# Kernel optimization log

Measured on AMD Instinct MI355X. Metric: run time of the kernel, lower is better.

## Reference

```python
import jax, jax.numpy as jnp
import numpy as np

B, S, D, H, MLP = 2, 2048, 1024, 16, 4096
DH = D // H
EPS_LN = 1e-6
KERNEL_EPS = 1e-3  # fast_attention generalized kernel_epsilon


def layer_norm(x, scale, bias):
    m = jnp.mean(x, axis=-1, keepdims=True)
    v = jnp.mean(jnp.square(x - m), axis=-1, keepdims=True)
    return (x - m) * jax.lax.rsqrt(v + EPS_LN) * scale + bias


def performer_causal_attention(q, k, v):
    """FAVOR+ generalized attention (deterministic relu features), causal.

    q,k,v: [B,S,H,DH]. phi(x) = relu(x) + eps. Linear-time via prefix sums:
      out_i = phi(q_i) . cumsum_j<=i phi(k_j) v_j^T / (phi(q_i) . cumsum phi(k_j))
    """
    phi_q = jax.nn.relu(q) + KERNEL_EPS          # [B,S,H,M]
    phi_k = jax.nn.relu(k) + KERNEL_EPS          # [B,S,H,M]
    kv = jnp.cumsum(jnp.einsum('bshm,bshd->bshmd', phi_k, v), axis=1)  # [B,S,H,M,DH]
    num = jnp.einsum('bshm,bshmd->bshd', phi_q, kv)
    den = jnp.einsum('bshm,bshm->bsh', phi_q, jnp.cumsum(phi_k, axis=1))
    return num / den[..., None]


def setup_inputs() -> dict:
    key = jax.random.key(0)
    ks = jax.random.split(key, 7)
    def w(k, shape, scale):
        return jax.random.normal(k, shape, jnp.float32) * scale
    s_in = 1.0 / np.sqrt(D)
    return {
        'inputs': jax.random.normal(ks[0], (B, S, D), jnp.float32),
        'ln1_scale': jnp.ones((D,), jnp.float32),
        'ln1_bias': jnp.zeros((D,), jnp.float32),
        'wq': w(ks[1], (D, H, DH), s_in),
        'wk': w(ks[2], (D, H, DH), s_in),
        'wv': w(ks[3], (D, H, DH), s_in),
        'wo': w(ks[4], (H, DH, D), s_in),
        'ln2_scale': jnp.ones((D,), jnp.float32),
        'ln2_bias': jnp.zeros((D,), jnp.float32),
        'w1': w(ks[5], (D, MLP), s_in),
        'b1': jnp.zeros((MLP,), jnp.float32),
        'w2': w(ks[6], (MLP, D), 1.0 / np.sqrt(MLP)),
        'b2': jnp.zeros((D,), jnp.float32),
    }


def reference(inputs, ln1_scale, ln1_bias, wq, wk, wv, wo,
              ln2_scale, ln2_bias, w1, b1, w2, b2):
    # pre-LN self-attention (Performer FAVOR+ generalized, causal)
    x = layer_norm(inputs, ln1_scale, ln1_bias)
    q = jnp.einsum('bsd,dhm->bshm', x, wq)
    k = jnp.einsum('bsd,dhm->bshm', x, wk)
    v = jnp.einsum('bsd,dhm->bshm', x, wv)
    attn = performer_causal_attention(q, k, v)          # [B,S,H,DH]
    attn_out = jnp.einsum('bshm,hmd->bsd', attn, wo)    # output projection
    x = attn_out + inputs                               # residual
    # pre-LN MLP block
    y = layer_norm(x, ln2_scale, ln2_bias)
    y = jax.nn.gelu(y @ w1 + b1) @ w2 + b2
    return x + y
```

## Files before the change

### kernel.cpp

```cpp
#include <hip/hip_runtime.h>
#include <math.h>
#include <stdint.h>

typedef __bf16 bf16;
typedef bf16  bf16x8 __attribute__((ext_vector_type(8)));
typedef float f32x4  __attribute__((ext_vector_type(4)));

constexpr int Bb  = 2;
constexpr int Ss  = 2048;
constexpr int Dd  = 1024;
constexpr int Hh  = 16;
constexpr int DHh = 64;
constexpr int MLPd = 4096;
constexpr int ROWS = Bb * Ss;
constexpr int NC  = Ss / 64;
constexpr int BH  = Bb * Hh;
constexpr float EPS_LN = 1e-6f;
constexpr float KEPS   = 1e-3f;

__device__ __forceinline__ void async_copy16(const bf16* g, bf16* l) {
    __builtin_amdgcn_global_load_lds(
        (__attribute__((address_space(1))) void*)g,
        (__attribute__((address_space(3))) void*)l,
        16, 0, 0);
}

__device__ __forceinline__ int swz64(int row, int col) {
    return row * 64 + (((col >> 3) ^ row) & 7) * 8 + (col & 7);
}

template <typename T>
__global__ __launch_bounds__(256) void ln_kernel(const T* __restrict__ x,
                                                 const float* __restrict__ scale,
                                                 const float* __restrict__ bias,
                                                 bf16* __restrict__ out)
{
    const int row = blockIdx.x;
    const T* xr = x + (size_t)row * Dd;
    const int c0 = threadIdx.x * 4;
    float vals[4];
    float sum = 0.f, sumsq = 0.f;
#pragma unroll
    for (int i = 0; i < 4; i++) {
        float v = (float)xr[c0 + i];
        vals[i] = v;
        sum += v;
        sumsq += v * v;
    }
#pragma unroll
    for (int off = 32; off > 0; off >>= 1) {
        sum   += __shfl_down(sum, off);
        sumsq += __shfl_down(sumsq, off);
    }
    __shared__ float ssum[4], ssq[4];
    const int wave = threadIdx.x >> 6;
    if ((threadIdx.x & 63) == 0) { ssum[wave] = sum; ssq[wave] = sumsq; }
    __syncthreads();
    const float tot   = ssum[0] + ssum[1] + ssum[2] + ssum[3];
    const float totsq = ssq[0] + ssq[1] + ssq[2] + ssq[3];
    const float mean = tot * (1.f / Dd);
    const float var  = totsq * (1.f / Dd) - mean * mean;
    const float r = rsqrtf(var + EPS_LN);
    bf16* orow = out + (size_t)row * Dd;
#pragma unroll
    for (int i = 0; i < 4; i++)
        orow[c0 + i] = (bf16)((vals[i] - mean) * r * scale[c0 + i] + bias[c0 + i]);
}

__global__ __launch_bounds__(256) void convert_T(const float* __restrict__ in,
                                                 bf16* __restrict__ out,
                                                 int K, int N)
{
    __shared__ float tile[32][33];
    const int k0 = blockIdx.y * 32, n0 = blockIdx.x * 32;
    const int tx = threadIdx.x & 31, ty = threadIdx.x >> 5;
#pragma unroll
    for (int i = 0; i < 32; i += 8)
        tile[ty + i][tx] = in[(size_t)(k0 + ty + i) * N + n0 + tx];
    __syncthreads();
#pragma unroll
    for (int i = 0; i < 32; i += 8)
        out[(size_t)(n0 + ty + i) * K + k0 + tx] = (bf16)tile[tx][ty + i];
}

__global__ __launch_bounds__(256) void convert_T4(const float* __restrict__ s0,
                                                  const float* __restrict__ s1,
                                                  const float* __restrict__ s2,
                                                  const float* __restrict__ s3,
                                                  bf16* __restrict__ d0,
                                                  bf16* __restrict__ d1,
                                                  bf16* __restrict__ d2,
                                                  bf16* __restrict__ d3)
{
    const float* in  = (blockIdx.z == 0) ? s0 : (blockIdx.z == 1) ? s1
                     : (blockIdx.z == 2) ? s2 : s3;
    bf16* out        = (blockIdx.z == 0) ? d0 : (blockIdx.z == 1) ? d1
                     : (blockIdx.z == 2) ? d2 : d3;
    __shared__ float tile[32][33];
    const int k0 = blockIdx.y * 32, n0 = blockIdx.x * 32;
    const int tx = threadIdx.x & 31, ty = threadIdx.x >> 5;
#pragma unroll
    for (int i = 0; i < 32; i += 8)
        tile[ty + i][tx] = in[(size_t)(k0 + ty + i) * 1024 + n0 + tx];
    __syncthreads();
#pragma unroll
    for (int i = 0; i < 32; i += 8)
        out[(size_t)(n0 + ty + i) * 1024 + k0 + tx] = (bf16)tile[tx][ty + i];
}

enum { EP_QKV = 0, EP_NONE = 1, EP_RES = 2, EP_GELU = 3, EP_BIAS_RES = 4 };

template <int TN, int BK, int NDIM, int KDIM, int MODE>
__global__ __launch_bounds__(256) void mfma_gemm(const bf16* __restrict__ A,
                                                 const bf16* __restrict__ BT,
                                                 void* __restrict__ Cout,
                                                 const float* __restrict__ bias,
                                                 const void* __restrict__ res,
                                                 bf16* __restrict__ out2,
                                                 bf16* __restrict__ out3)
{
    constexpr int WCT = TN / 2;
    constexpr int NJ  = TN / 32;
    constexpr int NS  = BK / 32;
    constexpr int CPR = BK / 8;
    constexpr int RPI = 2048 / BK;
    constexpr int GRIDY = 32;
    constexpr int RPX = GRIDY / 8;
    __shared__ bf16 As[128 * BK];
    __shared__ bf16 Bs[TN * BK];
    const int t = threadIdx.x;
    const int wave = t >> 6, lane = t & 63;

    const int bid = blockIdx.x;
    const int xcd = bid & 7, idx = bid >> 3;
    const int row0 = (xcd * RPX + (idx & (RPX - 1))) * 128;
    const int col0 = (idx / RPX) * TN;

    const int wr = wave >> 1, wc = wave & 1;

    const int srow = t / CPR;
    const int gch  = (t % CPR) ^ (srow & 7);
    const int sdst = t * 8;

    const bf16* gA = A  + (size_t)(row0 + srow) * KDIM + gch * 8;
    const bf16* gB = BT + (size_t)(col0 + srow) * KDIM + gch * 8;

    const int m = lane & 15, quad = lane >> 4;
    const int mx7 = m & 7;

    f32x4 acc[4][NJ] = {};

    for (int k0 = 0; k0 < KDIM; k0 += BK) {
        __syncthreads();
#pragma unroll
        for (int i = 0; i < 128 / RPI; i++)
            async_copy16(gA + (size_t)i * RPI * KDIM, &As[i * 2048 + sdst]);
#pragma unroll
        for (int i = 0; i < TN / RPI; i++)
            async_copy16(gB + (size_t)i * RPI * KDIM, &Bs[i * 2048 + sdst]);
        __syncthreads();

#pragma unroll
        for (int s = 0; s < NS; s++) {
            const int pco = ((s * 4 + quad) ^ mx7) * 8;
            bf16x8 aF[4], bF[NJ];
#pragma unroll
            for (int i = 0; i < 4; i++)
                aF[i] = *(const bf16x8*)&As[(wr * 64 + i * 16 + m) * BK + pco];
#pragma unroll
            for (int j = 0; j < NJ; j++)
                bF[j] = *(const bf16x8*)&Bs[(wc * WCT + j * 16 + m) * BK + pco];
#pragma unroll
            for (int i = 0; i < 4; i++)
#pragma unroll
                for (int j = 0; j < NJ; j++)
                    acc[i][j] = __builtin_amdgcn_mfma_f32_16x16x32_bf16(
                        aF[i], bF[j], acc[i][j], 0, 0, 0);
        }
        gA += BK;
        gB += BK;
    }

    bf16* qkv_dst = nullptr;
    int col_base = col0;
    bool do_phi = false;
    if constexpr (MODE == EP_QKV) {
        const int third = col0 >> 10;
        qkv_dst = (third == 0) ? (bf16*)Cout : (third == 1) ? out2 : out3;
        col_base = col0 & 1023;
        do_phi = (third < 2);
    }

#pragma unroll
    for (int i = 0; i < 4; i++) {
#pragma unroll
        for (int j = 0; j < NJ; j++) {
#pragma unroll
            for (int r = 0; r < 4; r++) {
                const int row = row0 + wr * 64 + i * 16 + quad * 4 + r;
                const int col = col0 + wc * WCT + j * 16 + m;
                float val = acc[i][j][r];
                if constexpr (MODE == EP_QKV) {
                    const int lc = col_base + wc * WCT + j * 16 + m;
                    if (do_phi) val = fmaxf(val, 0.f) + KEPS;
                    qkv_dst[(size_t)row * 1024 + lc] = (bf16)val;
                } else if constexpr (MODE == EP_NONE) {
                    ((bf16*)Cout)[(size_t)row * NDIM + col] = (bf16)val;
                } else if constexpr (MODE == EP_RES) {
                    val += ((const float*)res)[(size_t)row * NDIM + col];
                    ((bf16*)Cout)[(size_t)row * NDIM + col] = (bf16)val;
                } else if constexpr (MODE == EP_GELU) {
                    val += bias[col];
                    const float u = 0.7978845608028654f * (val + 0.044715f * val * val * val);
                    const float e = __expf(2.f * u);
                    val = val * (1.f - 1.f / (e + 1.f));
                    ((bf16*)Cout)[(size_t)row * NDIM + col] = (bf16)val;
                } else {
                    val += bias[col] + (float)((const bf16*)res)[(size_t)row * NDIM + col];
                    ((float*)Cout)[(size_t)row * NDIM + col] = val;
                }
            }
        }
    }
}

__global__ __launch_bounds__(256) void chunk_kv_kernel(const bf16* __restrict__ phik,
                                                       const bf16* __restrict__ v,
                                                       bf16* __restrict__ kvs,
                                                       float* __restrict__ ksums)
{
    const int c = blockIdx.x, bh = blockIdx.y;
    const int b = bh >> 4, h = bh & 15;
    __shared__ bf16 Kt[64 * 64];
    __shared__ bf16 Vt[64 * 64];
    const int t = threadIdx.x;
    const int wave = t >> 6, lane = t & 63;
    const int m16 = lane & 15, quad = lane >> 4;
    const int wr = wave >> 1, wc = wave & 1;
    const int f = t & 63, s4 = t >> 6;

#pragma unroll
    for (int i = 0; i < 16; i++) {
        const int s = s4 + 4 * i;
        const size_t g = ((size_t)((b * Ss + c * 64 + s) * Hh + h)) * DHh + f;
        Kt[swz64(f, s)] = phik[g];
        Vt[swz64(f, s)] = v[g];
    }
    __syncthreads();

    f32x4 acc[2][2] = {};
#pragma unroll
    for (int ks = 0; ks < 2; ks++) {
        bf16x8 aF[2], bF[2];
#pragma unroll
        for (int i = 0; i < 2; i++)
            aF[i] = *(const bf16x8*)&Kt[swz64(wr * 32 + i * 16 + m16, ks * 32 + quad * 8)];
#pragma unroll
        for (int j = 0; j < 2; j++)
            bF[j] = *(const bf16x8*)&Vt[swz64(wc * 32 + j * 16 + m16, ks * 32 + quad * 8)];
#pragma unroll
        for (int i = 0; i < 2; i++)
#pragma unroll
            for (int j = 0; j < 2; j++)
                acc[i][j] = __builtin_amdgcn_mfma_f32_16x16x32_bf16(
                    aF[i], bF[j], acc[i][j], 0, 0, 0);
    }

    const size_t base = ((size_t)bh * NC + c) * 4096;
#pragma unroll
    for (int i = 0; i < 2; i++)
#pragma unroll
        for (int j = 0; j < 2; j++)
#pragma unroll
            for (int r = 0; r < 4; r++) {
                const int mrow = wr * 32 + i * 16 + quad * 4 + r;
                const int dcol = wc * 32 + j * 16 + m16;
                kvs[base + mrow * 64 + dcol] = (bf16)acc[i][j][r];
            }

    if (t < 64) {
        float s_ = 0.f;
#pragma unroll
        for (int p = 0; p < 8; p++) {
            bf16x8 k8 = *(const bf16x8*)&Kt[t * 64 + p * 8];
#pragma unroll
            for (int e = 0; e < 8; e++) s_ += (float)k8[e];
        }
        ksums[((size_t)bh * NC + c) * 64 + t] = s_;
    }
}

__global__ __launch_bounds__(256) void scan_kernel(bf16* __restrict__ kvs,
                                                   float* __restrict__ ksums)
{
    const int e  = blockIdx.x * 256 + threadIdx.x;
    const int bh = blockIdx.y;
    float run = 0.f;
#pragma unroll 4
    for (int c = 0; c < NC; c++) {
        const size_t idx = ((size_t)bh * NC + c) * 4096 + e;
        const float val = (float)kvs[idx];
        kvs[idx] = (bf16)run;
        run += val;
    }
    if (blockIdx.x == 0 && threadIdx.x < 64) {
        float r = 0.f;
        for (int c = 0; c < NC; c++) {
            const size_t idx = ((size_t)bh * NC + c) * 64 + threadIdx.x;
            const float val = ksums[idx];
            ksums[idx] = r;
            r += val;
        }
    }
}

__global__ __launch_bounds__(256) void attn_out_kernel(const bf16* __restrict__ phiq,
                                                       const bf16* __restrict__ phik,
                                                       const bf16* __restrict__ v,
                                                       const bf16* __restrict__ kvs,
                                                       const float* __restrict__ ksums,
                                                       bf16* __restrict__ attn)
{
    const int c = blockIdx.x, bh = blockIdx.y;
    const int b = bh >> 4, h = bh & 15;
    __shared__ bf16 Qs [64 * 64];
    __shared__ bf16 KVb[64 * 64];
    __shared__ bf16 Sm [64 * 64];
    __shared__ bf16 KVt[64 * 64];
    __shared__ float ksm[64], den[64];
    const int t = threadIdx.x;
    const int wave = t >> 6, lane = t & 63;
    const int m16 = lane & 15, quad = lane >> 4;
    const int wr = wave >> 1, wc = wave & 1;
    const int f = t & 63, s4 = t >> 6;

#pragma unroll
    for (int i = 0; i < 16; i++) {
        const int s = s4 + 4 * i;
        const size_t g = ((size_t)((b * Ss + c * 64 + s) * Hh + h)) * DHh + f;
        Qs [swz64(s, f)] = phiq[g];
        KVb[swz64(s, f)] = phik[g];
    }
    if (t < 64) ksm[t] = ksums[((size_t)bh * NC + c) * 64 + t];
    __syncthreads();

    f32x4 sacc[2][2] = {};
#pragma unroll
    for (int ks = 0; ks < 2; ks++) {
        bf16x8 aF[2], bF[2];
#pragma unroll
        for (int i = 0; i < 2; i++)
            aF[i] = *(const bf16x8*)&Qs [swz64(wr * 32 + i * 16 + m16, ks * 32 + quad * 8)];
#pragma unroll
        for (int j = 0; j < 2; j++)
            bF[j] = *(const bf16x8*)&KVb[swz64(wc * 32 + j * 16 + m16, ks * 32 + quad * 8)];
#pragma unroll
        for (int i = 0; i < 2; i++)
#pragma unroll
            for (int j = 0; j < 2; j++)
                sacc[i][j] = __builtin_amdgcn_mfma_f32_16x16x32_bf16(
                    aF[i], bF[j], sacc[i][j], 0, 0, 0);
    }
#pragma unroll
    for (int i = 0; i < 2; i++)
#pragma unroll
        for (int j = 0; j < 2; j++)
#pragma unroll
            for (int r = 0; r < 4; r++) {
                const int row = wr * 32 + i * 16 + quad * 4 + r;
                const int col = wc * 32 + j * 16 + m16;
                Sm[swz64(row, col)] = (bf16)((col <= row) ? sacc[i][j][r] : 0.f);
            }
    __syncthreads();

#pragma unroll
    for (int i = 0; i < 16; i++) {
        const int s = s4 + 4 * i;
        const size_t g = ((size_t)((b * Ss + c * 64 + s) * Hh + h)) * DHh + f;
        KVb[swz64(f, s)] = v[g];
    }
    {
        const size_t base = ((size_t)bh * NC + c) * 4096;
#pragma unroll
        for (int i = 0; i < 16; i++) {
            const int e = t + 256 * i;
            KVt[swz64(e & 63, e >> 6)] = kvs[base + e];
        }
    }
    __syncthreads();

    if (t < 64) {
        float d_ = 0.f;
#pragma unroll
        for (int p = 0; p < 8; p++) {
            const int gc = (p ^ (t & 7)) * 8;
            bf16x8 q8 = *(const bf16x8*)&Qs[t * 64 + p * 8];
            bf16x8 s8 = *(const bf16x8*)&Sm[t * 64 + p * 8];
#pragma unroll
            for (int e = 0; e < 8; e++)
                d_ += (float)q8[e] * ksm[gc + e] + (float)s8[e];
        }
        den[t] = d_;
    }

    f32x4 oacc[2][2] = {};
#pragma unroll
    for (int ks = 0; ks < 2; ks++) {
        bf16x8 aF[2], bF[2];
#pragma unroll
        for (int i = 0; i < 2; i++)
            aF[i] = *(const bf16x8*)&Sm [swz64(wr * 32 + i * 16 + m16, ks * 32 + quad * 8)];
#pragma unroll
        for (int j = 0; j < 2; j++)
            bF[j] = *(const bf16x8*)&KVb[swz64(wc * 32 + j * 16 + m16, ks * 32 + quad * 8)];
#pragma unroll
        for (int i = 0; i < 2; i++)
#pragma unroll
            for (int j = 0; j < 2; j++)
                oacc[i][j] = __builtin_amdgcn_mfma_f32_16x16x32_bf16(
                    aF[i], bF[j], oacc[i][j], 0, 0, 0);
    }
#pragma unroll
    for (int ks = 0; ks < 2; ks++) {
        bf16x8 aF[2], bF[2];
#pragma unroll
        for (int i = 0; i < 2; i++)
            aF[i] = *(const bf16x8*)&Qs [swz64(wr * 32 + i * 16 + m16, ks * 32 + quad * 8)];
#pragma unroll
        for (int j = 0; j < 2; j++)
            bF[j] = *(const bf16x8*)&KVt[swz64(wc * 32 + j * 16 + m16, ks * 32 + quad * 8)];
#pragma unroll
        for (int i = 0; i < 2; i++)
#pragma unroll
            for (int j = 0; j < 2; j++)
                oacc[i][j] = __builtin_amdgcn_mfma_f32_16x16x32_bf16(
                    aF[i], bF[j], oacc[i][j], 0, 0, 0);
    }
    __syncthreads();

#pragma unroll
    for (int i = 0; i < 2; i++) {
#pragma unroll
        for (int r = 0; r < 4; r++) {
            const int row = wr * 32 + i * 16 + quad * 4 + r;
            const float dinv = 1.f / den[row];
#pragma unroll
            for (int j = 0; j < 2; j++) {
                const int col = wc * 32 + j * 16 + m16;
                attn[((size_t)((b * Ss + c * 64 + row) * Hh + h)) * DHh + col] =
                    (bf16)(oacc[i][j][r] * dinv);
            }
        }
    }
}

extern "C" void kernel_launch(void* const* d_in, const int* in_sizes, int n_in,
                              void* d_out, int out_size, void* d_ws, size_t ws_size,
                              hipStream_t stream)
{
    const float* inputs    = (const float*)d_in[0];
    const float* ln1_scale = (const float*)d_in[1];
    const float* ln1_bias  = (const float*)d_in[2];
    const float* wq        = (const float*)d_in[3];
    const float* wk        = (const float*)d_in[4];
    const float* wv        = (const float*)d_in[5];
    const float* wo        = (const float*)d_in[6];
    const float* ln2_scale = (const float*)d_in[7];
    const float* ln2_bias  = (const float*)d_in[8];
    const float* w1        = (const float*)d_in[9];
    const float* b1        = (const float*)d_in[10];
    const float* w2        = (const float*)d_in[11];
    const float* b2        = (const float*)d_in[12];
    float* out = (float*)d_out;

    char* ws = (char*)d_ws;
    bf16*  xln   = (bf16*)ws;
    bf16*  q     = (bf16*)(ws + (8ull  << 20));
    bf16*  k     = (bf16*)(ws + (16ull << 20));
    bf16*  v     = (bf16*)(ws + (24ull << 20));
    bf16*  kvs   = (bf16*)(ws + (32ull << 20));
    bf16*  x2    = (bf16*)(ws + (48ull << 20));
    float* ksums = (float*)(ws + (64ull << 20));
    bf16*  wqT   = (bf16*)(ws + (64ull << 20) + (1ull << 18));
    bf16*  wkT   = wqT + 1024 * 1024;
    bf16*  wvT   = wkT + 1024 * 1024;
    bf16*  woT   = wvT + 1024 * 1024;
    bf16*  w1T   = woT + 1024 * 1024;
    bf16*  w2T   = w1T + 4096 * 1024;
    bf16*  attn  = xln;
    bf16*  yln   = q;
    bf16*  hbuf  = k;

    convert_T4<<<dim3(32, 32, 4), 256, 0, stream>>>(wq, wk, wv, wo, wqT, wkT, wvT, woT);
    convert_T<<<dim3(4096 / 32, 1024 / 32), 256, 0, stream>>>(w1, w1T, 1024, 4096);
    convert_T<<<dim3(1024 / 32, 4096 / 32), 256, 0, stream>>>(w2, w2T, 4096, 1024);

    ln_kernel<float><<<ROWS, 256, 0, stream>>>(inputs, ln1_scale, ln1_bias, xln);

    mfma_gemm<128, 64, 3072, 1024, EP_QKV><<<dim3(24 * 32), 256, 0, stream>>>(
        xln, wqT, q, nullptr, nullptr, k, v);

    {
        dim3 gridA(NC, BH);
        chunk_kv_kernel<<<gridA, 256, 0, stream>>>(k, v, kvs, ksums);
        scan_kernel<<<dim3(4096 / 256, BH), 256, 0, stream>>>(kvs, ksums);
        attn_out_kernel<<<gridA, 256, 0, stream>>>(q, k, v, kvs, ksums, attn);
    }

    mfma_gemm<64, 128, 1024, 1024, EP_RES><<<dim3(16 * 32), 256, 0, stream>>>(
        attn, woT, x2, nullptr, inputs, nullptr, nullptr);

    ln_kernel<bf16><<<ROWS, 256, 0, stream>>>(x2, ln2_scale, ln2_bias, yln);

    mfma_gemm<128, 64, 4096, 1024, EP_GELU><<<dim3(32 * 32), 256, 0, stream>>>(
        yln, w1T, hbuf, b1, nullptr, nullptr, nullptr);
    mfma_gemm<64, 128, 1024, 4096, EP_BIAS_RES><<<dim3(16 * 32), 256, 0, stream>>>(
        hbuf, w2T, out, b2, x2, nullptr, nullptr);
}
```

Measured before the change: 304.5 us.

## Merge weight transposes and first layernorm into one preprocessing launch; shrink GEMM BK

Merges the four weight-transpose launches and the first layernorm into one preprocessing kernel that dispatches on block index, and also writes a bf16 copy of the inputs. The attention output-projection residual now reads that bf16 copy instead of fp32 inputs, halving residual read traffic at some precision cost. The BK of the two N=1024 GEMMs is cut from 128 to 64, changing LDS use and occupancy. Fewer launches cut per-kernel overhead, but rounding the residual to bf16 adds error.

```diff
diff --git a/kernel.cpp b/kernel.cpp
--- a/kernel.cpp
+++ b/kernel.cpp
@@ -29,14 +29,92 @@
     return row * 64 + (((col >> 3) ^ row) & 7) * 8 + (col & 7);
 }
 
-template <typename T>
-__global__ __launch_bounds__(256) void ln_kernel(const T* __restrict__ x,
+__global__ __launch_bounds__(256) void preproc_kernel(
+    const float* __restrict__ inputs,
+    const float* __restrict__ ln1_scale, const float* __restrict__ ln1_bias,
+    bf16* __restrict__ xln, bf16* __restrict__ inp_bf,
+    const float* __restrict__ wq, const float* __restrict__ wk,
+    const float* __restrict__ wv, const float* __restrict__ wo,
+    bf16* __restrict__ wqT, bf16* __restrict__ wkT,
+    bf16* __restrict__ wvT, bf16* __restrict__ woT,
+    const float* __restrict__ w1, bf16* __restrict__ w1T,
+    const float* __restrict__ w2, bf16* __restrict__ w2T)
+{
+    __shared__ float tile[32][33];
+    __shared__ float ssum[4], ssq[4];
+    const int blk = blockIdx.x;
+    const int sector = blk >> 12;
+
+    if (sector == 0) {
+        const int row = blk;
+        const float* xr = inputs + (size_t)row * Dd;
+        const int c0 = threadIdx.x * 4;
+        float vals[4];
+        float sum = 0.f, sumsq = 0.f;
+#pragma unroll
+        for (int i = 0; i < 4; i++) {
+            float v = xr[c0 + i];
+            vals[i] = v;
+            sum += v;
+            sumsq += v * v;
+        }
+#pragma unroll
+        for (int off = 32; off > 0; off >>= 1) {
+            sum   += __shfl_down(sum, off);
+            sumsq += __shfl_down(sumsq, off);
+        }
+        const int wave = threadIdx.x >> 6;
+        if ((threadIdx.x & 63) == 0) { ssum[wave] = sum; ssq[wave] = sumsq; }
+        __syncthreads();
+        const float tot   = ssum[0] + ssum[1] + ssum[2] + ssum[3];
+        const float totsq = ssq[0] + ssq[1] + ssq[2] + ssq[3];
+        const float mean = tot * (1.f / Dd);
+        const float var  = totsq * (1.f / Dd) - mean * mean;
+        const float r = rsqrtf(var + EPS_LN);
+        bf16* orow = xln + (size_t)row * Dd;
+        bf16* irow = inp_bf + (size_t)row * Dd;
+#pragma unroll
+        for (int i = 0; i < 4; i++) {
+            irow[c0 + i] = (bf16)vals[i];
+            orow[c0 + i] = (bf16)((vals[i] - mean) * r * ln1_scale[c0 + i] + ln1_bias[c0 + i]);
+        }
+    } else {
+        const float* in; bf16* out; int K, N, bx, by;
+        if (sector == 1) {
+            const int local = blk - 4096;
+            const int z = local >> 10;
+            in  = (z == 0) ? wq : (z == 1) ? wk : (z == 2) ? wv : wo;
+            out = (z == 0) ? wqT : (z == 1) ? wkT : (z == 2) ? wvT : woT;
+            K = 1024; N = 1024;
+            bx = local & 31; by = (local >> 5) & 31;
+        } else if (sector == 2) {
+            const int local = blk - 8192;
+            in = w1; out = w1T; K = 1024; N = 4096;
+            bx = local & 127; by = local >> 7;
+        } else {
+            const int local = blk - 12288;
+            in = w2; out = w2T; K = 4096; N = 1024;
+            bx = local & 31; by = local >> 5;
+        }
+        const int k0 = by * 32, n0 = bx * 32;
+        const int tx = threadIdx.x & 31, ty = threadIdx.x >> 5;
+#pragma unroll
+        for (int i = 0; i < 32; i += 8)
+            tile[ty + i][tx] = in[(size_t)(k0 + ty + i) * N + n0 + tx];
+        __syncthreads();
+#pragma unroll
+        for (int i = 0; i < 32; i += 8)
+            out[(size_t)(n0 + ty + i) * K + k0 + tx] = (bf16)tile[tx][ty + i];
+    }
+}
+
+__global__ __launch_bounds__(256) void ln_kernel(const bf16* __restrict__ x,
                                                  const float* __restrict__ scale,
                                                  const float* __restrict__ bias,
                                                  bf16* __restrict__ out)
 {
     const int row = blockIdx.x;
-    const T* xr = x + (size_t)row * Dd;
+    const bf16* xr = x + (size_t)row * Dd;
     const int c0 = threadIdx.x * 4;
     float vals[4];
     float sum = 0.f, sumsq = 0.f;
@@ -65,47 +143,6 @@
 #pragma unroll
     for (int i = 0; i < 4; i++)
         orow[c0 + i] = (bf16)((vals[i] - mean) * r * scale[c0 + i] + bias[c0 + i]);
-}
-
-__global__ __launch_bounds__(256) void convert_T(const float* __restrict__ in,
-                                                 bf16* __restrict__ out,
-                                                 int K, int N)
-{
-    __shared__ float tile[32][33];
-    const int k0 = blockIdx.y * 32, n0 = blockIdx.x * 32;
-    const int tx = threadIdx.x & 31, ty = threadIdx.x >> 5;
-#pragma unroll
-    for (int i = 0; i < 32; i += 8)
-        tile[ty + i][tx] = in[(size_t)(k0 + ty + i) * N + n0 + tx];
-    __syncthreads();
-#pragma unroll
-    for (int i = 0; i < 32; i += 8)
-        out[(size_t)(n0 + ty + i) * K + k0 + tx] = (bf16)tile[tx][ty + i];
-}
-
-__global__ __launch_bounds__(256) void convert_T4(const float* __restrict__ s0,
-                                                  const float* __restrict__ s1,
-                                                  const float* __restrict__ s2,
-                                                  const float* __restrict__ s3,
-                                                  bf16* __restrict__ d0,
-                                                  bf16* __restrict__ d1,
-                                                  bf16* __restrict__ d2,
-                                                  bf16* __restrict__ d3)
-{
-    const float* in  = (blockIdx.z == 0) ? s0 : (blockIdx.z == 1) ? s1
-                     : (blockIdx.z == 2) ? s2 : s3;
-    bf16* out        = (blockIdx.z == 0) ? d0 : (blockIdx.z == 1) ? d1
-                     : (blockIdx.z == 2) ? d2 : d3;
-    __shared__ float tile[32][33];
-    const int k0 = blockIdx.y * 32, n0 = blockIdx.x * 32;
-    const int tx = threadIdx.x & 31, ty = threadIdx.x >> 5;
-#pragma unroll
-    for (int i = 0; i < 32; i += 8)
-        tile[ty + i][tx] = in[(size_t)(k0 + ty + i) * 1024 + n0 + tx];
-    __syncthreads();
-#pragma unroll
-    for (int i = 0; i < 32; i += 8)
-        out[(size_t)(n0 + ty + i) * 1024 + k0 + tx] = (bf16)tile[tx][ty + i];
 }
 
 enum { EP_QKV = 0, EP_NONE = 1, EP_RES = 2, EP_GELU = 3, EP_BIAS_RES = 4 };
@@ -207,7 +244,7 @@
                 } else if constexpr (MODE == EP_NONE) {
                     ((bf16*)Cout)[(size_t)row * NDIM + col] = (bf16)val;
                 } else if constexpr (MODE == EP_RES) {
-                    val += ((const float*)res)[(size_t)row * NDIM + col];
+                    val += (float)((const bf16*)res)[(size_t)row * NDIM + col];
                     ((bf16*)Cout)[(size_t)row * NDIM + col] = (bf16)val;
                 } else if constexpr (MODE == EP_GELU) {
                     val += bias[col];
@@ -480,6 +517,7 @@
     bf16*  v     = (bf16*)(ws + (24ull << 20));
     bf16*  kvs   = (bf16*)(ws + (32ull << 20));
     bf16*  x2    = (bf16*)(ws + (48ull << 20));
+    bf16*  inp_bf= (bf16*)(ws + (56ull << 20));
     float* ksums = (float*)(ws + (64ull << 20));
     bf16*  wqT   = (bf16*)(ws + (64ull << 20) + (1ull << 18));
     bf16*  wkT   = wqT + 1024 * 1024;
@@ -491,11 +529,9 @@
     bf16*  yln   = q;
     bf16*  hbuf  = k;
 
-    convert_T4<<<dim3(32, 32, 4), 256, 0, stream>>>(wq, wk, wv, wo, wqT, wkT, wvT, woT);
-    convert_T<<<dim3(4096 / 32, 1024 / 32), 256, 0, stream>>>(w1, w1T, 1024, 4096);
-    convert_T<<<dim3(1024 / 32, 4096 / 32), 256, 0, stream>>>(w2, w2T, 4096, 1024);
-
-    ln_kernel<float><<<ROWS, 256, 0, stream>>>(inputs, ln1_scale, ln1_bias, xln);
+    preproc_kernel<<<16384, 256, 0, stream>>>(
+        inputs, ln1_scale, ln1_bias, xln, inp_bf,
+        wq, wk, wv, wo, wqT, wkT, wvT, woT, w1, w1T, w2, w2T);
 
     mfma_gemm<128, 64, 3072, 1024, EP_QKV><<<dim3(24 * 32), 256, 0, stream>>>(
         xln, wqT, q, nullptr, nullptr, k, v);
@@ -507,13 +543,13 @@
         attn_out_kernel<<<gridA, 256, 0, stream>>>(q, k, v, kvs, ksums, attn);
     }
 
-    mfma_gemm<64, 128, 1024, 1024, EP_RES><<<dim3(16 * 32), 256, 0, stream>>>(
-        attn, woT, x2, nullptr, inputs, nullptr, nullptr);
-
-    ln_kernel<bf16><<<ROWS, 256, 0, stream>>>(x2, ln2_scale, ln2_bias, yln);
+    mfma_gemm<64, 64, 1024, 1024, EP_RES><<<dim3(16 * 32), 256, 0, stream>>>(
+        attn, woT, x2, nullptr, inp_bf, nullptr, nullptr);
+
+    ln_kernel<<<ROWS, 256, 0, stream>>>(x2, ln2_scale, ln2_bias, yln);
 
     mfma_gemm<128, 64, 4096, 1024, EP_GELU><<<dim3(32 * 32), 256, 0, stream>>>(
         yln, w1T, hbuf, b1, nullptr, nullptr, nullptr);
-    mfma_gemm<64, 128, 1024, 4096, EP_BIAS_RES><<<dim3(16 * 32), 256, 0, stream>>>(
+    mfma_gemm<64, 64, 1024, 4096, EP_BIAS_RES><<<dim3(16 * 32), 256, 0, stream>>>(
         hbuf, w2T, out, b2, x2, nullptr, nullptr);
 }
```

New measurement: 303.1 us. No clear change (-0.5%).
